# Kernel tuning notes

Measured on AMD Instinct MI355X. Metric: run time of the kernel, lower is better.

Reference implementation:

```python
import jax, jax.numpy as jnp
import numpy as np

B, S, D, H = 4, 2048, 1024, 16
HD = D // H  # head_dim = 64


def setup_inputs() -> dict:
    key = jax.random.key(0)
    k1, k2, k3 = jax.random.split(key, 3)
    x = jax.random.normal(k1, (B, S, D), dtype=jnp.float32)
    W_attn = jax.random.normal(k2, (D, 3 * D), dtype=jnp.float32) * (1.0 / np.sqrt(D))
    b_attn = jnp.zeros((3 * D,), dtype=jnp.float32)
    W_proj = jax.random.normal(k3, (D, D), dtype=jnp.float32) * (1.0 / np.sqrt(D))
    b_proj = jnp.zeros((D,), dtype=jnp.float32)
    return {"x": x, "W_attn": W_attn, "b_attn": b_attn, "W_proj": W_proj, "b_proj": b_proj}


def reference(x, W_attn, b_attn, W_proj, b_proj):
    bsz, seq_len, d = x.shape
    n_head = H
    head_dim = d // n_head
    qkv = x @ W_attn + b_attn                      # [B,S,3D]
    q, k, v = jnp.split(qkv, 3, axis=-1)           # each [B,S,D]
    # -> [B,H,S,hd]
    q = q.reshape(bsz, seq_len, n_head, head_dim).transpose(0, 2, 1, 3)
    k = k.reshape(bsz, seq_len, n_head, head_dim).transpose(0, 2, 1, 3)
    v = v.reshape(bsz, seq_len, n_head, head_dim).transpose(0, 2, 1, 3)
    scale = 1.0 / np.sqrt(head_dim).astype(np.float32)
    att = jnp.einsum("bhqd,bhkd->bhqk", q, k) * scale  # [B,H,S,S]
    causal = jnp.tril(jnp.ones((seq_len, seq_len), dtype=bool))
    att = jnp.where(causal[None, None], att, jnp.float32(-jnp.inf))
    att = jax.nn.softmax(att, axis=-1)
    y = jnp.einsum("bhqk,bhkd->bhqd", att, v)       # [B,H,S,hd]
    y = y.transpose(0, 2, 1, 3).reshape(bsz, seq_len, d)
    return y @ W_proj + b_proj
```

## Files before the change

### kernel.cpp

```cpp
#include <hip/hip_runtime.h>

typedef __attribute__((ext_vector_type(8))) short short8;
typedef __attribute__((ext_vector_type(8))) __bf16 bf16x8;
typedef __attribute__((ext_vector_type(2))) __bf16 bf16x2;
typedef __attribute__((ext_vector_type(4))) float f32x4;
typedef __attribute__((ext_vector_type(2))) unsigned int uint2v;

#define LOG2E 1.44269504088896340736f

__device__ __forceinline__ unsigned short f2b(float f) {
  unsigned u = __builtin_bit_cast(unsigned, f);
  u += 0x7fffu + ((u >> 16) & 1u);
  return (unsigned short)(u >> 16);
}
__device__ __forceinline__ float b2f(unsigned short s) {
  unsigned u = (unsigned)s << 16;
  return __builtin_bit_cast(float, u);
}
__device__ __forceinline__ bf16x8 asbf(short8 s) { return __builtin_bit_cast(bf16x8, s); }

__device__ __forceinline__ void gl_lds16(const void* g, void* l) {
  __builtin_amdgcn_global_load_lds(
      (const __attribute__((address_space(1))) void*)g,
      (__attribute__((address_space(3))) void*)l, 16, 0, 0);
}

__device__ __forceinline__ unsigned lds_a(const void* p) {
  return (unsigned)(size_t)(__attribute__((address_space(3))) const void*)p;
}

__device__ __forceinline__ unsigned pk_bf16(float a, float b) {
  bf16x2 v;
  v[0] = (__bf16)a;
  v[1] = (__bf16)b;
  return __builtin_bit_cast(unsigned, v);
}

template <int N>
__device__ __forceinline__ void wait_vm() {
  if constexpr (N == 7) asm volatile("s_waitcnt vmcnt(7)" ::: "memory");
  else if constexpr (N == 6) asm volatile("s_waitcnt vmcnt(6)" ::: "memory");
  else if constexpr (N == 5) asm volatile("s_waitcnt vmcnt(5)" ::: "memory");
  else asm volatile("s_waitcnt vmcnt(0)" ::: "memory");
}

__global__ void k_cvt_bf16(const float* __restrict__ x, unsigned short* __restrict__ o, int n) {
  int i = (blockIdx.x * 256 + threadIdx.x) * 4;
  if (i >= n) return;
  float4 v = *(const float4*)(x + i);
  ushort4 r;
  r.x = f2b(v.x); r.y = f2b(v.y); r.z = f2b(v.z); r.w = f2b(v.w);
  *(ushort4*)(o + i) = r;
}

__global__ void k_transpose_bf16(const float* __restrict__ W, unsigned short* __restrict__ Wt,
                                 int R, int C) {
  __shared__ float tile[64][65];
  const int tc = blockIdx.x, tr = blockIdx.y;
  const int r0 = tr * 64, c0 = tc * 64;
  for (int it = 0; it < 16; ++it) {
    int lin = it * 256 + threadIdx.x;
    int r = lin >> 6, c = lin & 63;
    tile[r][c] = W[(size_t)(r0 + r) * C + c0 + c];
  }
  __syncthreads();
  for (int it = 0; it < 16; ++it) {
    int lin = it * 256 + threadIdx.x;
    int orr = lin >> 6, oc = lin & 63;
    Wt[(size_t)(c0 + orr) * R + r0 + oc] = f2b(tile[oc][orr]);
  }
}

template <int BNW, bool OUT_BF16>
__global__ __launch_bounds__(512)
void k_gemm256(const unsigned short* __restrict__ A, const unsigned short* __restrict__ Bt,
               const float* __restrict__ bias, void* __restrict__ Cp,
               int M, int N, int K) {
  constexpr int BN = BNW * 4;
  constexpr int NR = BNW / 16;
  __shared__ unsigned short lds[2][(256 + BN) * 64];

  const int tid = threadIdx.x;
  const int wv = tid >> 6, lane = tid & 63;
  const int g = lane >> 4, l15 = lane & 15;
  const int wr = wv >> 2, wc = wv & 3;

  const int ntn = N / BN;
  const int nwg = gridDim.x;
  const int bid = blockIdx.x;
  const int cpx = nwg >> 3;
  const int swz = (bid & 7) * cpx + (bid >> 3);
  const int tm = swz / ntn, tn = swz % ntn;

  const unsigned short* Ab = A + (size_t)(tm * 256) * K;
  const unsigned short* Bb = Bt + (size_t)(tn * BN) * K;

  const int NT = K >> 6, NI = NT >> 1;

  auto As = [&](int buf) -> char* { return (char*)&lds[buf][0]; };
  auto Bs = [&](int buf) -> char* { return (char*)&lds[buf][256 * 64]; };

  auto stageB = [&](int buf, int t) {
#pragma unroll
    for (int it = 0; it < NR; ++it) {
      int cidx = it * 8 + wv;
      int row = cidx * 8 + (lane >> 3);
      int sc = (lane & 7) ^ (row & 7);
      gl_lds16(Bb + (size_t)row * K + t * 64 + sc * 8, Bs(buf) + cidx * 1024 + lane * 16);
    }
  };
  auto stageA = [&](int buf, int t, int q) {
    int row0 = (wv < 4) ? (q * 32 + wv * 8) : (128 + q * 32 + (wv - 4) * 8);
    int row = row0 + (lane >> 3);
    int sc = (lane & 7) ^ (row & 7);
    gl_lds16(Ab + (size_t)row * K + t * 64 + sc * 8, As(buf) + row0 * 128 + lane * 16);
  };

  auto rdA = [&](int buf, int q, int ms, int kh) -> short8 {
    int row = wr * 128 + q * 32 + ms * 16 + l15;
    int ch = (kh * 4 + g) ^ (row & 7);
    return *(const short8*)(As(buf) + row * 128 + ch * 16);
  };
  auto rdB = [&](int buf, int n, int kh) -> short8 {
    int row = wc * BNW + n * 16 + l15;
    int ch = (kh * 4 + g) ^ (row & 7);
    return *(const short8*)(Bs(buf) + row * 128 + ch * 16);
  };

  f32x4 acc[8][NR] = {};
  short8 bfr[NR][2];

  stageB(0, 0);
#pragma unroll
  for (int q = 0; q < 4; ++q) stageA(0, 0, q);
  stageB(1, 1);
#pragma unroll
  for (int q = 0; q < 3; ++q) stageA(1, 1, q);
  wait_vm<NR + 3>();
  __builtin_amdgcn_s_barrier();

  for (int i = 0; i < NI; ++i) {
    const int t0 = 2 * i;
#pragma unroll
    for (int half = 0; half < 2; ++half) {
#pragma unroll
      for (int q = 0; q < 4; ++q) {
        short8 afr[2][2];
#pragma unroll
        for (int ms = 0; ms < 2; ++ms)
#pragma unroll
          for (int kh = 0; kh < 2; ++kh) afr[ms][kh] = rdA(half, q, ms, kh);
        if (q == 0) {
#pragma unroll
          for (int n = 0; n < NR; ++n)
#pragma unroll
            for (int kh = 0; kh < 2; ++kh) bfr[n][kh] = rdB(half, n, kh);
        }
        if (half == 0) {
          if (q == 0) stageA(1, t0 + 1, 3);
          if (q == 1 && t0 + 2 < NT) { stageB(0, t0 + 2); stageA(0, t0 + 2, 0); }
          if (q == 2 && t0 + 2 < NT) stageA(0, t0 + 2, 1);
          if (q == 3 && t0 + 2 < NT) stageA(0, t0 + 2, 2);
        } else {
          if (q == 0 && t0 + 2 < NT) stageA(0, t0 + 2, 3);
          if (q == 1 && t0 + 3 < NT) stageB(1, t0 + 3);
          if (q == 2 && t0 + 3 < NT) stageA(1, t0 + 3, 0);
          if (q == 3 && t0 + 3 < NT) { stageA(1, t0 + 3, 1); stageA(1, t0 + 3, 2); }
        }
        __builtin_amdgcn_s_barrier();
        asm volatile("s_waitcnt lgkmcnt(0)" ::: "memory");
        __builtin_amdgcn_sched_barrier(0);
        __builtin_amdgcn_s_setprio(1);
#pragma unroll
        for (int n = 0; n < NR; ++n)
#pragma unroll
          for (int ms = 0; ms < 2; ++ms)
#pragma unroll
            for (int kh = 0; kh < 2; ++kh)
              acc[q * 2 + ms][n] = __builtin_amdgcn_mfma_f32_16x16x32_bf16(
                  asbf(afr[ms][kh]), asbf(bfr[n][kh]), acc[q * 2 + ms][n], 0, 0, 0);
        __builtin_amdgcn_s_setprio(0);
        if (q == 3) {
          const bool more = (half == 0) ? (t0 + 2 < NT) : (t0 + 3 < NT);
          if (more) wait_vm<NR + 3>();
          else      wait_vm<0>();
        }
        __builtin_amdgcn_s_barrier();
      }
    }
  }

  const int crow0 = tm * 256 + wr * 128 + g * 4;
  const int ccol0 = tn * BN + wc * BNW + l15;
#pragma unroll
  for (int n = 0; n < NR; ++n) {
    int col = ccol0 + n * 16;
    float bv = bias[col];
#pragma unroll
    for (int mq = 0; mq < 8; ++mq)
#pragma unroll
      for (int j = 0; j < 4; ++j) {
        int row = crow0 + mq * 16 + j;
        float v = acc[mq][n][j] + bv;
        if constexpr (OUT_BF16)
          ((unsigned short*)Cp)[(size_t)row * N + col] = f2b(v);
        else
          ((float*)Cp)[(size_t)row * N + col] = v;
      }
  }
}

__global__ __launch_bounds__(512)
void k_attn(const unsigned short* __restrict__ qkv, unsigned short* __restrict__ y) {
  constexpr int SEQ = 2048, TD = 3072, DM = 1024;
  __shared__ unsigned short Kl[2][4096];
  __shared__ unsigned short Vl[2][4096];
  __shared__ unsigned short Pl[8][2048];

  const int f = blockIdx.x;
  const int wrk = (f & 7) * 32 + (f >> 3);
  const int bh = wrk >> 2, pr = wrk & 3;
  const int b = bh >> 4, h = bh & 15;
  const int tid = threadIdx.x;
  const int lane = tid & 63, w = tid >> 6;
  const int g = lane >> 4, l15 = lane & 15;

  const size_t base = (size_t)b * SEQ * TD + h * 64;
  const unsigned short* Kg0 = qkv + base + 1024;
  const unsigned short* Vg0 = qkv + base + 2048;

  short8 onesb;
#pragma unroll
  for (int i = 0; i < 8; ++i) onesb[i] = (short)0x3F80;

  auto stage = [&](int buf, int c) {
    const unsigned short* Kg = Kg0 + (size_t)(c * 64) * TD;
    const unsigned short* Vg = Vg0 + (size_t)(c * 64) * TD;
    const int j = tid;
    int r = j >> 3, cc = j & 7;
    int cck = cc ^ (r & 7);
    gl_lds16(Kg + (size_t)r * TD + cck * 8, (char*)Kl[buf] + j * 16);
    int kv = ((j >> 1) & 3) | (((j >> 5) & 1) << 2) | (((j >> 3) & 3) << 3) |
             (((j >> 6) & 1) << 5);
    int d0 = ((j >> 7) << 4) | ((j & 1) << 3);
    gl_lds16(Vg + (size_t)kv * TD + d0, (char*)Vl[buf] + j * 16);
  };

  char* pw = (char*)Pl + w * 4096;

  for (int half = 0; half < 2; ++half) {
    const int qt = half ? (7 - pr) : pr;
    const int q0 = qt * 256;
    const int qw = w * 32;

    short8 qf[2][2];
#pragma unroll
    for (int qg = 0; qg < 2; ++qg) {
      const unsigned short* qrow = qkv + base + (size_t)(q0 + qw + qg * 16 + l15) * TD;
#pragma unroll
      for (int kh = 0; kh < 2; ++kh) {
        short8 t = *(const short8*)(qrow + kh * 32 + g * 8);
#pragma unroll
        for (int i = 0; i < 8; ++i)
          t[i] = (short)f2b(b2f((unsigned short)t[i]) * (0.125f * LOG2E));
        qf[qg][kh] = t;
      }
    }

    f32x4 o[2][4] = {};
    f32x4 ol[2] = {};

    const int nch = 4 * (qt + 1);
    int cur = 0;
    stage(0, 0);
    for (int c = 0; c < nch; ++c) {
      if (c + 1 < nch) {
        stage(cur ^ 1, c + 1);
        asm volatile("s_waitcnt vmcnt(2)" ::: "memory");
      } else {
        asm volatile("s_waitcnt vmcnt(0)" ::: "memory");
      }
      __builtin_amdgcn_s_barrier();

      f32x4 sv[2][4];
      __builtin_amdgcn_s_setprio(1);
#pragma unroll
      for (int ff = 0; ff < 4; ++ff) {
        int kv = ff * 16 + l15;
        short8 kf0 = *(const short8*)((const char*)Kl[cur] + kv * 128 + ((g) ^ (kv & 7)) * 16);
        short8 kf1 = *(const short8*)((const char*)Kl[cur] + kv * 128 + ((4 + g) ^ (kv & 7)) * 16);
#pragma unroll
        for (int qg = 0; qg < 2; ++qg) {
          f32x4 s = {};
          s = __builtin_amdgcn_mfma_f32_16x16x32_bf16(asbf(kf0), asbf(qf[qg][0]), s, 0, 0, 0);
          s = __builtin_amdgcn_mfma_f32_16x16x32_bf16(asbf(kf1), asbf(qf[qg][1]), s, 0, 0, 0);
          sv[qg][ff] = s;
        }
      }
      __builtin_amdgcn_s_setprio(0);

      const int crel = c - 4 * qt;
      if (crel >= 0) {
#pragma unroll
        for (int qg = 0; qg < 2; ++qg)
#pragma unroll
          for (int ff = 0; ff < 4; ++ff)
#pragma unroll
            for (int r = 0; r < 4; ++r)
              if (crel * 64 + ff * 16 + g * 4 + r > qw + qg * 16 + l15)
                sv[qg][ff][r] = -128.f;
      }

#pragma unroll
      for (int qg = 0; qg < 2; ++qg)
#pragma unroll
        for (int ff = 0; ff < 4; ++ff) {
          float p0 = __builtin_amdgcn_exp2f(sv[qg][ff][0]);
          float p1 = __builtin_amdgcn_exp2f(sv[qg][ff][1]);
          float p2 = __builtin_amdgcn_exp2f(sv[qg][ff][2]);
          float p3 = __builtin_amdgcn_exp2f(sv[qg][ff][3]);
          unsigned w0 = pk_bf16(p0, p1);
          unsigned w1 = pk_bf16(p2, p3);
          unsigned long long pk = (unsigned long long)w0 | ((unsigned long long)w1 << 32);
          int off = qg * 2048 + ((l15 * 128 + ff * 32 + g * 8) ^ ((l15 & 7) << 4));
          *(unsigned long long*)(pw + off) = pk;
        }

      const unsigned vaddr = lds_a((const char*)Vl[cur] + g * 128 + l15 * 8);
#pragma unroll
      for (int kvh = 0; kvh < 2; ++kvh) {
        uint2v t0[4], t1[4];
#pragma unroll
        for (int n = 0; n < 4; ++n) {
          asm volatile("ds_read_b64_tr_b16 %0, %1 offset:%2"
                       : "=v"(t0[n]) : "v"(vaddr), "i"(n * 2048 + kvh * 1024));
          asm volatile("ds_read_b64_tr_b16 %0, %1 offset:%2"
                       : "=v"(t1[n]) : "v"(vaddr), "i"(n * 2048 + kvh * 1024 + 512));
        }
        asm volatile("s_waitcnt lgkmcnt(0)" ::: "memory");
        __builtin_amdgcn_sched_barrier(0);
        __builtin_amdgcn_s_setprio(1);
#pragma unroll
        for (int qg = 0; qg < 2; ++qg) {
          short8 pa = *(const short8*)(pw + qg * 2048 +
                                       ((l15 * 128 + kvh * 64 + g * 16) ^ ((l15 & 7) << 4)));
#pragma unroll
          for (int n = 0; n < 4; ++n) {
            union { uint2v u[2]; short8 s; } uu;
            uu.u[0] = t0[n]; uu.u[1] = t1[n];
            o[qg][n] = __builtin_amdgcn_mfma_f32_16x16x32_bf16(asbf(pa), asbf(uu.s),
                                                               o[qg][n], 0, 0, 0);
          }
          ol[qg] = __builtin_amdgcn_mfma_f32_16x16x32_bf16(asbf(pa), asbf(onesb),
                                                           ol[qg], 0, 0, 0);
        }
        __builtin_amdgcn_s_setprio(0);
      }

      __builtin_amdgcn_s_barrier();
      cur ^= 1;
    }

#pragma unroll
    for (int qg = 0; qg < 2; ++qg) {
      float lj[4];
#pragma unroll
      for (int j = 0; j < 4; ++j) lj[j] = 1.f / ol[qg][j];
#pragma unroll
      for (int n = 0; n < 4; ++n)
#pragma unroll
        for (int j = 0; j < 4; ++j) {
          int row = q0 + qw + qg * 16 + g * 4 + j;
          int col = h * 64 + n * 16 + l15;
          y[(size_t)(b * SEQ + row) * DM + col] = f2b(o[qg][n][j] * lj[j]);
        }
    }
  }
}

extern "C" void kernel_launch(void* const* d_in, const int* in_sizes, int n_in,
                              void* d_out, int out_size, void* d_ws, size_t ws_size,
                              hipStream_t stream) {
  const float* x = (const float*)d_in[0];
  const float* W_attn = (const float*)d_in[1];
  const float* b_attn = (const float*)d_in[2];
  const float* W_proj = (const float*)d_in[3];
  const float* b_proj = (const float*)d_in[4];
  float* out = (float*)d_out;

  const int B = 4, S = 2048, D = 1024;
  const int M = B * S;
  const int TD = 3 * D;

  char* ws = (char*)d_ws;
  unsigned short* qkvb = (unsigned short*)ws;
  unsigned short* xb = (unsigned short*)(ws + (size_t)M * TD * 2);
  unsigned short* Wat = (unsigned short*)(ws + (size_t)M * TD * 2 + (size_t)M * D * 2);
  unsigned short* Wpt = Wat + (size_t)TD * D;

  k_cvt_bf16<<<(M * D) / 1024, 256, 0, stream>>>(x, xb, M * D);
  k_transpose_bf16<<<dim3(TD / 64, D / 64), 256, 0, stream>>>(W_attn, Wat, D, TD);
  k_transpose_bf16<<<dim3(D / 64, D / 64), 256, 0, stream>>>(W_proj, Wpt, D, D);

  k_gemm256<48, true><<<(M / 256) * (TD / 192), 512, 0, stream>>>(xb, Wat, b_attn, qkvb, M, TD, D);
  k_attn<<<256, 512, 0, stream>>>(qkvb, xb);
  k_gemm256<32, false><<<(M / 256) * (D / 128), 512, 0, stream>>>(xb, Wpt, b_proj, out, M, D, D);
}
```

Measured before the change: 164.7 us.

## Restructure GEMM mainloop to BK=32 with smaller LDS and higher occupancy

The GEMM K-tile shrinks from 64 to 32, and the A and B tiles are re-laid out in LDS with a 4-chunk XOR swizzle. This cuts LDS per block to 64KB so that launch_bounds(512,4) can request more resident waves. The complex quarter-staged prefetch schedule becomes a simpler per-K-step loop: A for t+1 is prefetched into the other buffer, and B for t+2 is staged mid-iteration. The change doubles the number of barriers per unit of K work and presses on registers, and the B staging for t+2 into the buffer currently being read depends on barrier placement to stay correct.

```diff
diff --git a/kernel.cpp b/kernel.cpp
--- a/kernel.cpp
+++ b/kernel.cpp
@@ -34,14 +34,6 @@
   v[0] = (__bf16)a;
   v[1] = (__bf16)b;
   return __builtin_bit_cast(unsigned, v);
-}
-
-template <int N>
-__device__ __forceinline__ void wait_vm() {
-  if constexpr (N == 7) asm volatile("s_waitcnt vmcnt(7)" ::: "memory");
-  else if constexpr (N == 6) asm volatile("s_waitcnt vmcnt(6)" ::: "memory");
-  else if constexpr (N == 5) asm volatile("s_waitcnt vmcnt(5)" ::: "memory");
-  else asm volatile("s_waitcnt vmcnt(0)" ::: "memory");
 }
 
 __global__ void k_cvt_bf16(const float* __restrict__ x, unsigned short* __restrict__ o, int n) {
@@ -72,13 +64,13 @@
 }
 
 template <int BNW, bool OUT_BF16>
-__global__ __launch_bounds__(512)
+__global__ __launch_bounds__(512, 4)
 void k_gemm256(const unsigned short* __restrict__ A, const unsigned short* __restrict__ Bt,
                const float* __restrict__ bias, void* __restrict__ Cp,
                int M, int N, int K) {
   constexpr int BN = BNW * 4;
   constexpr int NR = BNW / 16;
-  __shared__ unsigned short lds[2][(256 + BN) * 64];
+  __shared__ unsigned short lds[2][512 * 32];
 
   const int tid = threadIdx.x;
   const int wv = tid >> 6, lane = tid & 63;
@@ -95,99 +87,100 @@
   const unsigned short* Ab = A + (size_t)(tm * 256) * K;
   const unsigned short* Bb = Bt + (size_t)(tn * BN) * K;
 
-  const int NT = K >> 6, NI = NT >> 1;
+  const int NT = K >> 5;
 
   auto As = [&](int buf) -> char* { return (char*)&lds[buf][0]; };
-  auto Bs = [&](int buf) -> char* { return (char*)&lds[buf][256 * 64]; };
-
+  auto Bs = [&](int buf) -> char* { return (char*)&lds[buf][256 * 32]; };
+
+  auto stageA = [&](int buf, int t) {
+#pragma unroll
+    for (int it = 0; it < 2; ++it) {
+      int cidx = it * 512 + tid;
+      int row = cidx >> 2, c8 = cidx & 3;
+      int sc = c8 ^ ((row >> 1) & 3);
+      gl_lds16(Ab + (size_t)row * K + t * 32 + sc * 8, As(buf) + cidx * 16);
+    }
+  };
   auto stageB = [&](int buf, int t) {
 #pragma unroll
-    for (int it = 0; it < NR; ++it) {
-      int cidx = it * 8 + wv;
-      int row = cidx * 8 + (lane >> 3);
-      int sc = (lane & 7) ^ (row & 7);
-      gl_lds16(Bb + (size_t)row * K + t * 64 + sc * 8, Bs(buf) + cidx * 1024 + lane * 16);
+    for (int it = 0; it < 2; ++it) {
+      int cidx = it * 512 + tid;
+      int row = cidx >> 2, c8 = cidx & 3;
+      int sc = c8 ^ ((row >> 1) & 3);
+      int grow = (row < BN) ? row : 0;
+      gl_lds16(Bb + (size_t)grow * K + t * 32 + sc * 8, Bs(buf) + cidx * 16);
     }
   };
-  auto stageA = [&](int buf, int t, int q) {
-    int row0 = (wv < 4) ? (q * 32 + wv * 8) : (128 + q * 32 + (wv - 4) * 8);
-    int row = row0 + (lane >> 3);
-    int sc = (lane & 7) ^ (row & 7);
-    gl_lds16(Ab + (size_t)row * K + t * 64 + sc * 8, As(buf) + row0 * 128 + lane * 16);
+
+  auto rdA = [&](int buf, int ms) -> short8 {
+    int row = wr * 128 + ms * 16 + l15;
+    int ch = g ^ ((row >> 1) & 3);
+    return *(const short8*)(As(buf) + row * 64 + ch * 16);
   };
-
-  auto rdA = [&](int buf, int q, int ms, int kh) -> short8 {
-    int row = wr * 128 + q * 32 + ms * 16 + l15;
-    int ch = (kh * 4 + g) ^ (row & 7);
-    return *(const short8*)(As(buf) + row * 128 + ch * 16);
+  auto rdB = [&](int buf, int n) -> short8 {
+    int row = wc * BNW + n * 16 + l15;
+    int ch = g ^ ((row >> 1) & 3);
+    return *(const short8*)(Bs(buf) + row * 64 + ch * 16);
   };
-  auto rdB = [&](int buf, int n, int kh) -> short8 {
-    int row = wc * BNW + n * 16 + l15;
-    int ch = (kh * 4 + g) ^ (row & 7);
-    return *(const short8*)(Bs(buf) + row * 128 + ch * 16);
-  };
 
   f32x4 acc[8][NR] = {};
-  short8 bfr[NR][2];
-
+
+  stageA(0, 0);
   stageB(0, 0);
-#pragma unroll
-  for (int q = 0; q < 4; ++q) stageA(0, 0, q);
   stageB(1, 1);
-#pragma unroll
-  for (int q = 0; q < 3; ++q) stageA(1, 1, q);
-  wait_vm<NR + 3>();
+  asm volatile("s_waitcnt vmcnt(2)" ::: "memory");
   __builtin_amdgcn_s_barrier();
 
-  for (int i = 0; i < NI; ++i) {
-    const int t0 = 2 * i;
-#pragma unroll
-    for (int half = 0; half < 2; ++half) {
-#pragma unroll
-      for (int q = 0; q < 4; ++q) {
-        short8 afr[2][2];
-#pragma unroll
-        for (int ms = 0; ms < 2; ++ms)
-#pragma unroll
-          for (int kh = 0; kh < 2; ++kh) afr[ms][kh] = rdA(half, q, ms, kh);
-        if (q == 0) {
-#pragma unroll
-          for (int n = 0; n < NR; ++n)
-#pragma unroll
-            for (int kh = 0; kh < 2; ++kh) bfr[n][kh] = rdB(half, n, kh);
-        }
-        if (half == 0) {
-          if (q == 0) stageA(1, t0 + 1, 3);
-          if (q == 1 && t0 + 2 < NT) { stageB(0, t0 + 2); stageA(0, t0 + 2, 0); }
-          if (q == 2 && t0 + 2 < NT) stageA(0, t0 + 2, 1);
-          if (q == 3 && t0 + 2 < NT) stageA(0, t0 + 2, 2);
-        } else {
-          if (q == 0 && t0 + 2 < NT) stageA(0, t0 + 2, 3);
-          if (q == 1 && t0 + 3 < NT) stageB(1, t0 + 3);
-          if (q == 2 && t0 + 3 < NT) stageA(1, t0 + 3, 0);
-          if (q == 3 && t0 + 3 < NT) { stageA(1, t0 + 3, 1); stageA(1, t0 + 3, 2); }
-        }
-        __builtin_amdgcn_s_barrier();
-        asm volatile("s_waitcnt lgkmcnt(0)" ::: "memory");
-        __builtin_amdgcn_sched_barrier(0);
-        __builtin_amdgcn_s_setprio(1);
-#pragma unroll
-        for (int n = 0; n < NR; ++n)
-#pragma unroll
-          for (int ms = 0; ms < 2; ++ms)
-#pragma unroll
-            for (int kh = 0; kh < 2; ++kh)
-              acc[q * 2 + ms][n] = __builtin_amdgcn_mfma_f32_16x16x32_bf16(
-                  asbf(afr[ms][kh]), asbf(bfr[n][kh]), acc[q * 2 + ms][n], 0, 0, 0);
-        __builtin_amdgcn_s_setprio(0);
-        if (q == 3) {
-          const bool more = (half == 0) ? (t0 + 2 < NT) : (t0 + 3 < NT);
-          if (more) wait_vm<NR + 3>();
-          else      wait_vm<0>();
-        }
-        __builtin_amdgcn_s_barrier();
-      }
-    }
+  for (int t = 0; t < NT; ++t) {
+    const int buf = t & 1, nbuf = buf ^ 1;
+    short8 bfr[NR], a0, a1;
+
+    if (t + 1 < NT) stageA(nbuf, t + 1);
+#pragma unroll
+    for (int n = 0; n < NR; ++n) bfr[n] = rdB(buf, n);
+    a0 = rdA(buf, 0);
+    a1 = rdA(buf, 1);
+    asm volatile("s_waitcnt lgkmcnt(0)" ::: "memory");
+    __builtin_amdgcn_sched_barrier(0);
+    __builtin_amdgcn_s_barrier();
+    __builtin_amdgcn_s_setprio(1);
+#pragma unroll
+    for (int n = 0; n < NR; ++n) {
+      acc[0][n] = __builtin_amdgcn_mfma_f32_16x16x32_bf16(asbf(a0), asbf(bfr[n]), acc[0][n], 0, 0, 0);
+      acc[1][n] = __builtin_amdgcn_mfma_f32_16x16x32_bf16(asbf(a1), asbf(bfr[n]), acc[1][n], 0, 0, 0);
+    }
+    a0 = rdA(buf, 2);
+    a1 = rdA(buf, 3);
+#pragma unroll
+    for (int n = 0; n < NR; ++n) {
+      acc[2][n] = __builtin_amdgcn_mfma_f32_16x16x32_bf16(asbf(a0), asbf(bfr[n]), acc[2][n], 0, 0, 0);
+      acc[3][n] = __builtin_amdgcn_mfma_f32_16x16x32_bf16(asbf(a1), asbf(bfr[n]), acc[3][n], 0, 0, 0);
+    }
+    __builtin_amdgcn_s_setprio(0);
+
+    if (t + 2 < NT) stageB(buf, t + 2);
+    a0 = rdA(buf, 4);
+    a1 = rdA(buf, 5);
+    asm volatile("s_waitcnt lgkmcnt(0)" ::: "memory");
+    __builtin_amdgcn_sched_barrier(0);
+    __builtin_amdgcn_s_barrier();
+    __builtin_amdgcn_s_setprio(1);
+#pragma unroll
+    for (int n = 0; n < NR; ++n) {
+      acc[4][n] = __builtin_amdgcn_mfma_f32_16x16x32_bf16(asbf(a0), asbf(bfr[n]), acc[4][n], 0, 0, 0);
+      acc[5][n] = __builtin_amdgcn_mfma_f32_16x16x32_bf16(asbf(a1), asbf(bfr[n]), acc[5][n], 0, 0, 0);
+    }
+    a0 = rdA(buf, 6);
+    a1 = rdA(buf, 7);
+#pragma unroll
+    for (int n = 0; n < NR; ++n) {
+      acc[6][n] = __builtin_amdgcn_mfma_f32_16x16x32_bf16(asbf(a0), asbf(bfr[n]), acc[6][n], 0, 0, 0);
+      acc[7][n] = __builtin_amdgcn_mfma_f32_16x16x32_bf16(asbf(a1), asbf(bfr[n]), acc[7][n], 0, 0, 0);
+    }
+    __builtin_amdgcn_s_setprio(0);
+    if (t + 2 < NT) asm volatile("s_waitcnt vmcnt(2)" ::: "memory");
+    else            asm volatile("s_waitcnt vmcnt(0)" ::: "memory");
+    __builtin_amdgcn_s_barrier();
   }
 
   const int crow0 = tm * 256 + wr * 128 + g * 4;
```

New measurement: 191.2 us. 1.16x slower.
